# Kernel optimization log

Measured on AMD Instinct MI355X. Metric: run time of the kernel, lower is better.

## Reference

```python
import jax, jax.numpy as jnp
import numpy as np

EPS = 1e-6

def sparsemax(z):
    # z: [B, N]; sparsemax along last axis (Martins & Astudillo 2016)
    N = z.shape[-1]
    z_sorted = jnp.flip(jnp.sort(z, axis=-1), axis=-1)          # descending
    cs = jnp.cumsum(z_sorted, axis=-1)                            # [B, N]
    k = jnp.arange(1, N + 1, dtype=z.dtype)                       # [N]
    support = (1.0 + k * z_sorted) > cs                           # [B, N]
    k_sel = jnp.sum(support, axis=-1).astype(jnp.int32)           # [B]
    cs_k = jnp.take_along_axis(cs, (k_sel - 1)[:, None], axis=-1)[:, 0]
    tau = (cs_k - 1.0) / k_sel.astype(z.dtype)                    # [B]
    return jnp.maximum(z - tau[:, None], 0.0)

def _l2norm(x, axis):
    n = jnp.linalg.norm(x, axis=axis, keepdims=True)
    return x / jnp.maximum(n, EPS)

def setup_inputs() -> dict:
    key = jax.random.key(0)
    ks = jax.random.split(key, 6)
    B, N, D, OUT = 64, 4096, 1024, 1000
    D_IN, D_HID = 2 * D, 4 * D
    enc = jax.random.normal(ks[0], (B, D), dtype=jnp.float32)
    mem = jax.random.normal(ks[1], (B, N, D), dtype=jnp.float32)
    s1 = 1.0 / np.sqrt(D_IN)
    s2 = 1.0 / np.sqrt(D_HID)
    W1 = jax.random.uniform(ks[2], (D_HID, D_IN), jnp.float32, -s1, s1)
    b1 = jax.random.uniform(ks[3], (D_HID,), jnp.float32, -s1, s1)
    W2 = jax.random.uniform(ks[4], (OUT, D_HID), jnp.float32, -s2, s2)
    b2 = jax.random.uniform(ks[5], (OUT,), jnp.float32, -s2, s2)
    return {"encoder_output": enc, "memory_set": mem, "W1": W1, "b1": b1, "W2": W2, "b2": b2}

def reference(encoder_output, memory_set, W1, b1, W2, b2):
    # cosine distance: 1 - cos_sim
    xn = _l2norm(encoder_output, axis=-1)                         # [B, D]
    yn = _l2norm(memory_set, axis=-1)                             # [B, N, D]
    dist = 1.0 - jnp.einsum('bd,bnd->bn', xn, yn)                 # [B, N]
    content_weights = sparsemax(-dist)                            # [B, N]
    memory_vector = jnp.einsum('bn,bnd->bd', content_weights, memory_set)
    h = jnp.concatenate([encoder_output, memory_vector], axis=1)  # [B, 2D]
    h = jax.nn.relu(h @ W1.T + b1)
    return h @ W2.T + b2
```

## Files before the change

kernel.cpp:

```cpp
#include <hip/hip_runtime.h>
#include <cstdint>
#include <cstddef>

#define B_    64
#define N_    4096
#define D_    1024
#define DIN   2048
#define DHID  4096
#define OUT_N 1000
#define EPSF  1e-6f

__global__ void k_enc(const float* __restrict__ enc, float* __restrict__ cat,
                      float* __restrict__ inv_enc) {
  int b = blockIdx.x, tid = threadIdx.x;
  const float4* er = (const float4*)(enc + (size_t)b * D_);
  float4 v = er[tid];
  float ss = v.x*v.x + v.y*v.y + v.z*v.z + v.w*v.w;
  #pragma unroll
  for (int o = 32; o > 0; o >>= 1) ss += __shfl_xor(ss, o, 64);
  __shared__ float sb[4];
  if ((tid & 63) == 0) sb[tid >> 6] = ss;
  __syncthreads();
  if (tid == 0) {
    float t = sb[0] + sb[1] + sb[2] + sb[3];
    inv_enc[b] = 1.0f / fmaxf(sqrtf(t), EPSF);
  }
  ((float4*)(cat + (size_t)b * DIN))[tid] = v;
}

__global__ void k_cos(const float* __restrict__ enc, const float* __restrict__ mem,
                      const float* __restrict__ inv_enc, float* __restrict__ z) {
  int tid  = threadIdx.x;
  int lane = tid & 63;
  int r    = blockIdx.x * 4 + (tid >> 6);
  int b    = r >> 12;
  const float4* mr = (const float4*)mem + (size_t)r * 256;
  const float4* er = (const float4*)enc + (size_t)b * 256;
  float dot = 0.f, ss = 0.f;
  #pragma unroll
  for (int j = 0; j < 4; ++j) {
    float4 m = mr[j * 64 + lane];
    float4 e = er[j * 64 + lane];
    dot += e.x*m.x + e.y*m.y + e.z*m.z + e.w*m.w;
    ss  += m.x*m.x + m.y*m.y + m.z*m.z + m.w*m.w;
  }
  #pragma unroll
  for (int o = 32; o > 0; o >>= 1) {
    dot += __shfl_xor(dot, o, 64);
    ss  += __shfl_xor(ss,  o, 64);
  }
  if (lane == 0) z[r] = dot * inv_enc[b] / fmaxf(sqrtf(ss), EPSF);
}

__global__ void k_sparsemax(const float* __restrict__ z, int* __restrict__ idxl,
                            float* __restrict__ wl, int* __restrict__ cnt) {
  int b = blockIdx.x, tid = threadIdx.x;
  const float* zr = z + (size_t)b * N_;
  float zv[16];
  #pragma unroll
  for (int j = 0; j < 16; ++j) zv[j] = zr[j * 256 + tid];

  __shared__ float sb[4];
  __shared__ float sb2[4];

  float mx = -1e30f;
  #pragma unroll
  for (int j = 0; j < 16; ++j) mx = fmaxf(mx, zv[j]);
  #pragma unroll
  for (int o = 32; o > 0; o >>= 1) mx = fmaxf(mx, __shfl_xor(mx, o, 64));
  if ((tid & 63) == 0) sb[tid >> 6] = mx;
  __syncthreads();
  mx = fmaxf(fmaxf(sb[0], sb[1]), fmaxf(sb[2], sb[3]));
  __syncthreads();

  float lo = mx - 1.0f, hi = mx;
  for (int it = 0; it < 40; ++it) {
    float mid = 0.5f * (lo + hi);
    float s = 0.f;
    #pragma unroll
    for (int j = 0; j < 16; ++j) {
      float d = zv[j] - mid;
      s += (d > 0.f) ? d : 0.f;
    }
    #pragma unroll
    for (int o = 32; o > 0; o >>= 1) s += __shfl_xor(s, o, 64);
    if ((tid & 63) == 0) sb[tid >> 6] = s;
    __syncthreads();
    s = sb[0] + sb[1] + sb[2] + sb[3];
    __syncthreads();
    if (s >= 1.0f) lo = mid; else hi = mid;
  }
  float mid = 0.5f * (lo + hi);

  float c = 0.f, s = 0.f;
  #pragma unroll
  for (int j = 0; j < 16; ++j) {
    if (zv[j] > mid) { c += 1.0f; s += zv[j]; }
  }
  #pragma unroll
  for (int o = 32; o > 0; o >>= 1) {
    c += __shfl_xor(c, o, 64);
    s += __shfl_xor(s, o, 64);
  }
  if ((tid & 63) == 0) { sb[tid >> 6] = c; sb2[tid >> 6] = s; }
  __syncthreads();
  c = sb[0] + sb[1] + sb[2] + sb[3];
  s = sb2[0] + sb2[1] + sb2[2] + sb2[3];
  float tau = (s - 1.0f) / fmaxf(c, 1.0f);

  __shared__ int scnt;
  if (tid == 0) scnt = 0;
  __syncthreads();
  #pragma unroll
  for (int j = 0; j < 16; ++j) {
    float w = zv[j] - tau;
    if (w > 0.f) {
      int p = atomicAdd(&scnt, 1);
      idxl[(size_t)b * N_ + p] = j * 256 + tid;
      wl[(size_t)b * N_ + p]   = w;
    }
  }
  __syncthreads();
  if (tid == 0) cnt[b] = scnt;
}

__global__ void k_memvec(const float* __restrict__ mem, const int* __restrict__ idxl,
                         const float* __restrict__ wl, const int* __restrict__ cnt,
                         float* __restrict__ cat) {
  int b = blockIdx.x, tid = threadIdx.x;
  int nnz = cnt[b];
  __shared__ int   sidx[256];
  __shared__ float sw[256];
  float4 acc = make_float4(0.f, 0.f, 0.f, 0.f);
  const float4* mb = (const float4*)mem + (size_t)b * N_ * 256;
  for (int c0 = 0; c0 < nnz; c0 += 256) {
    int c = nnz - c0; if (c > 256) c = 256;
    if (tid < c) {
      sidx[tid] = idxl[(size_t)b * N_ + c0 + tid];
      sw[tid]   = wl[(size_t)b * N_ + c0 + tid];
    }
    __syncthreads();
    #pragma unroll 4
    for (int i = 0; i < c; ++i) {
      float  w = sw[i];
      float4 r = mb[(size_t)sidx[i] * 256 + tid];
      acc.x += w * r.x; acc.y += w * r.y; acc.z += w * r.z; acc.w += w * r.w;
    }
    __syncthreads();
  }
  ((float4*)(cat + (size_t)b * DIN + D_))[tid] = acc;
}

__global__ void k_gemm1(const float* __restrict__ X, const float* __restrict__ W,
                        float* __restrict__ hp) {
  int nt = blockIdx.x, kt = blockIdx.y, tid = threadIdx.x;
  __shared__ float Xs[16][68];
  __shared__ float Ws[16][68];
  int row = tid >> 2, c4 = (tid & 3) * 4;
  int tm = (tid & 15) * 4, tn = (tid >> 4) * 4;
  float acc[4][4] = {};
  const float* Xp = X + (size_t)row * DIN + c4;
  const float* Wp = W + ((size_t)nt * 64 + row) * DIN + c4;
  int kend = kt * 512 + 512;
  for (int k0 = kt * 512; k0 < kend; k0 += 16) {
    float4 xv = *(const float4*)(Xp + k0);
    float4 wv = *(const float4*)(Wp + k0);
    __syncthreads();
    Xs[c4+0][row] = xv.x; Xs[c4+1][row] = xv.y; Xs[c4+2][row] = xv.z; Xs[c4+3][row] = xv.w;
    Ws[c4+0][row] = wv.x; Ws[c4+1][row] = wv.y; Ws[c4+2][row] = wv.z; Ws[c4+3][row] = wv.w;
    __syncthreads();
    #pragma unroll
    for (int kk = 0; kk < 16; ++kk) {
      float a0 = Xs[kk][tm+0], a1 = Xs[kk][tm+1], a2 = Xs[kk][tm+2], a3 = Xs[kk][tm+3];
      float b0 = Ws[kk][tn+0], b1 = Ws[kk][tn+1], b2 = Ws[kk][tn+2], b3 = Ws[kk][tn+3];
      acc[0][0] += a0*b0; acc[0][1] += a0*b1; acc[0][2] += a0*b2; acc[0][3] += a0*b3;
      acc[1][0] += a1*b0; acc[1][1] += a1*b1; acc[1][2] += a1*b2; acc[1][3] += a1*b3;
      acc[2][0] += a2*b0; acc[2][1] += a2*b1; acc[2][2] += a2*b2; acc[2][3] += a2*b3;
      acc[3][0] += a3*b0; acc[3][1] += a3*b1; acc[3][2] += a3*b2; acc[3][3] += a3*b3;
    }
  }
  float* o = hp + ((size_t)kt * 64 + tm) * DHID + nt * 64 + tn;
  #pragma unroll
  for (int i = 0; i < 4; ++i)
    *(float4*)(o + (size_t)i * DHID) = make_float4(acc[i][0], acc[i][1], acc[i][2], acc[i][3]);
}

__global__ void k_gemm2(const float* __restrict__ hp, const float* __restrict__ b1p,
                        const float* __restrict__ W2, float* __restrict__ op) {
  int nt = blockIdx.x, kt = blockIdx.y, tid = threadIdx.x;
  __shared__ float Xs[16][68];
  __shared__ float Ws[16][68];
  int row = tid >> 2, c4 = (tid & 3) * 4;
  int tm = (tid & 15) * 4, tn = (tid >> 4) * 4;
  int nbase = nt * 64;
  float acc[4][4] = {};
  int kend = kt * 256 + 256;
  for (int k0 = kt * 256; k0 < kend; k0 += 16) {
    int k = k0 + c4;
    float4 xv = *(const float4*)(b1p + k);
    #pragma unroll
    for (int p = 0; p < 4; ++p) {
      float4 h = *(const float4*)(hp + ((size_t)p * 64 + row) * DHID + k);
      xv.x += h.x; xv.y += h.y; xv.z += h.z; xv.w += h.w;
    }
    xv.x = fmaxf(xv.x, 0.f); xv.y = fmaxf(xv.y, 0.f);
    xv.z = fmaxf(xv.z, 0.f); xv.w = fmaxf(xv.w, 0.f);
    int n = nbase + row;
    float4 wv = make_float4(0.f, 0.f, 0.f, 0.f);
    if (n < OUT_N) wv = *(const float4*)(W2 + (size_t)n * DHID + k);
    __syncthreads();
    Xs[c4+0][row] = xv.x; Xs[c4+1][row] = xv.y; Xs[c4+2][row] = xv.z; Xs[c4+3][row] = xv.w;
    Ws[c4+0][row] = wv.x; Ws[c4+1][row] = wv.y; Ws[c4+2][row] = wv.z; Ws[c4+3][row] = wv.w;
    __syncthreads();
    #pragma unroll
    for (int kk = 0; kk < 16; ++kk) {
      float a0 = Xs[kk][tm+0], a1 = Xs[kk][tm+1], a2 = Xs[kk][tm+2], a3 = Xs[kk][tm+3];
      float b0 = Ws[kk][tn+0], b1 = Ws[kk][tn+1], b2 = Ws[kk][tn+2], b3 = Ws[kk][tn+3];
      acc[0][0] += a0*b0; acc[0][1] += a0*b1; acc[0][2] += a0*b2; acc[0][3] += a0*b3;
      acc[1][0] += a1*b0; acc[1][1] += a1*b1; acc[1][2] += a1*b2; acc[1][3] += a1*b3;
      acc[2][0] += a2*b0; acc[2][1] += a2*b1; acc[2][2] += a2*b2; acc[2][3] += a2*b3;
      acc[3][0] += a3*b0; acc[3][1] += a3*b1; acc[3][2] += a3*b2; acc[3][3] += a3*b3;
    }
  }
  float* o = op + ((size_t)kt * 64 + tm) * 1024 + nbase + tn;
  #pragma unroll
  for (int i = 0; i < 4; ++i)
    *(float4*)(o + (size_t)i * 1024) = make_float4(acc[i][0], acc[i][1], acc[i][2], acc[i][3]);
}

__global__ void k_out(const float* __restrict__ op, const float* __restrict__ b2p,
                      float* __restrict__ out) {
  int o = blockIdx.x * 256 + threadIdx.x;
  int b = blockIdx.y;
  if (o >= OUT_N) return;
  float s = b2p[o];
  #pragma unroll
  for (int kt = 0; kt < 16; ++kt) s += op[((size_t)kt * 64 + b) * 1024 + o];
  out[(size_t)b * OUT_N + o] = s;
}

extern "C" void kernel_launch(void* const* d_in, const int* in_sizes, int n_in,
                              void* d_out, int out_size, void* d_ws, size_t ws_size,
                              hipStream_t stream) {
  const float* enc = (const float*)d_in[0];
  const float* mem = (const float*)d_in[1];
  const float* W1  = (const float*)d_in[2];
  const float* b1  = (const float*)d_in[3];
  const float* W2  = (const float*)d_in[4];
  const float* b2  = (const float*)d_in[5];
  float* out = (float*)d_out;

  float* ws      = (float*)d_ws;
  float* inv_enc = ws;
  int*   cnt     = (int*)(ws + 64);
  float* z       = ws + 128;
  int*   idxl    = (int*)(ws + 128 + 262144);
  float* wl      = ws + 128 + 2 * 262144;
  float* cat     = ws + 128 + 3 * 262144;
  float* hp      = cat + 131072;
  float* op      = hp + 1048576;

  k_enc      <<<dim3(64),      dim3(256), 0, stream>>>(enc, cat, inv_enc);
  k_cos      <<<dim3(65536),   dim3(256), 0, stream>>>(enc, mem, inv_enc, z);
  k_sparsemax<<<dim3(64),      dim3(256), 0, stream>>>(z, idxl, wl, cnt);
  k_memvec   <<<dim3(64),      dim3(256), 0, stream>>>(mem, idxl, wl, cnt, cat);
  k_gemm1    <<<dim3(64, 4),   dim3(256), 0, stream>>>(cat, W1, hp);
  k_gemm2    <<<dim3(16, 16),  dim3(256), 0, stream>>>(hp, b1, W2, op);
  k_out      <<<dim3(4, 64),   dim3(256), 0, stream>>>(op, b2, out);
}
```

Measured before the change: 1.423 ms.

## Split GEMM1 K further, add separate bias-ReLU reduce, move enc norm to sparsemax

GEMM1 now splits K into eight slices instead of four, doubling grid size for better occupancy, and a new kernel reduces the partials, adds bias and applies ReLU once. GEMM2 then reads the final hidden activations directly instead of re-reducing partials per tile. The cosine kernel uses rsqrt and drops the per-row inv_enc load, with the encoder norm scale applied in sparsemax instead. memvec unroll goes from 4 to 8. The costs are an extra launch and more partial-sum traffic, plus slightly different eps clamping semantics.

```diff
diff --git a/kernel.cpp b/kernel.cpp
--- a/kernel.cpp
+++ b/kernel.cpp
@@ -10,8 +10,8 @@
 #define OUT_N 1000
 #define EPSF  1e-6f
 
-__global__ void k_enc(const float* __restrict__ enc, float* __restrict__ cat,
-                      float* __restrict__ inv_enc) {
+__global__ void k_prep(const float* __restrict__ enc, float* __restrict__ cat,
+                       float* __restrict__ inv_enc) {
   int b = blockIdx.x, tid = threadIdx.x;
   const float4* er = (const float4*)(enc + (size_t)b * D_);
   float4 v = er[tid];
@@ -29,7 +29,7 @@
 }
 
 __global__ void k_cos(const float* __restrict__ enc, const float* __restrict__ mem,
-                      const float* __restrict__ inv_enc, float* __restrict__ z) {
+                      float* __restrict__ z) {
   int tid  = threadIdx.x;
   int lane = tid & 63;
   int r    = blockIdx.x * 4 + (tid >> 6);
@@ -49,16 +49,22 @@
     dot += __shfl_xor(dot, o, 64);
     ss  += __shfl_xor(ss,  o, 64);
   }
-  if (lane == 0) z[r] = dot * inv_enc[b] / fmaxf(sqrtf(ss), EPSF);
-}
-
-__global__ void k_sparsemax(const float* __restrict__ z, int* __restrict__ idxl,
-                            float* __restrict__ wl, int* __restrict__ cnt) {
+  if (lane == 0) {
+    float inv = rsqrtf(ss);
+    inv = fminf(inv, 1.0f / EPSF);
+    z[r] = dot * inv;
+  }
+}
+
+__global__ void k_sparsemax(const float* __restrict__ z, const float* __restrict__ inv_enc,
+                            int* __restrict__ idxl, float* __restrict__ wl,
+                            int* __restrict__ cnt) {
   int b = blockIdx.x, tid = threadIdx.x;
   const float* zr = z + (size_t)b * N_;
+  float ie = inv_enc[b];
   float zv[16];
   #pragma unroll
-  for (int j = 0; j < 16; ++j) zv[j] = zr[j * 256 + tid];
+  for (int j = 0; j < 16; ++j) zv[j] = zr[j * 256 + tid] * ie;
 
   __shared__ float sb[4];
   __shared__ float sb2[4];
@@ -140,7 +146,7 @@
       sw[tid]   = wl[(size_t)b * N_ + c0 + tid];
     }
     __syncthreads();
-    #pragma unroll 4
+    #pragma unroll 8
     for (int i = 0; i < c; ++i) {
       float  w = sw[i];
       float4 r = mb[(size_t)sidx[i] * 256 + tid];
@@ -161,8 +167,8 @@
   float acc[4][4] = {};
   const float* Xp = X + (size_t)row * DIN + c4;
   const float* Wp = W + ((size_t)nt * 64 + row) * DIN + c4;
-  int kend = kt * 512 + 512;
-  for (int k0 = kt * 512; k0 < kend; k0 += 16) {
+  int kend = kt * 256 + 256;
+  for (int k0 = kt * 256; k0 < kend; k0 += 16) {
     float4 xv = *(const float4*)(Xp + k0);
     float4 wv = *(const float4*)(Wp + k0);
     __syncthreads();
@@ -185,29 +191,38 @@
     *(float4*)(o + (size_t)i * DHID) = make_float4(acc[i][0], acc[i][1], acc[i][2], acc[i][3]);
 }
 
-__global__ void k_gemm2(const float* __restrict__ hp, const float* __restrict__ b1p,
-                        const float* __restrict__ W2, float* __restrict__ op) {
+__global__ void k_hrelu(const float* __restrict__ hp, const float* __restrict__ b1p,
+                        float* __restrict__ h) {
+  int flat4 = blockIdx.x * 256 + threadIdx.x;
+  int k4 = flat4 & 1023;
+  float4 acc = ((const float4*)b1p)[k4];
+  #pragma unroll
+  for (int p = 0; p < 8; ++p) {
+    float4 v = ((const float4*)hp)[(size_t)p * 65536 + flat4];
+    acc.x += v.x; acc.y += v.y; acc.z += v.z; acc.w += v.w;
+  }
+  acc.x = fmaxf(acc.x, 0.f); acc.y = fmaxf(acc.y, 0.f);
+  acc.z = fmaxf(acc.z, 0.f); acc.w = fmaxf(acc.w, 0.f);
+  ((float4*)h)[flat4] = acc;
+}
+
+__global__ void k_gemm2(const float* __restrict__ h, const float* __restrict__ W2,
+                        float* __restrict__ op) {
   int nt = blockIdx.x, kt = blockIdx.y, tid = threadIdx.x;
   __shared__ float Xs[16][68];
   __shared__ float Ws[16][68];
   int row = tid >> 2, c4 = (tid & 3) * 4;
   int tm = (tid & 15) * 4, tn = (tid >> 4) * 4;
   int nbase = nt * 64;
+  int n = nbase + row;
   float acc[4][4] = {};
+  const float* Xp = h + (size_t)row * DHID + c4;
+  const float* Wp = W2 + (size_t)n * DHID + c4;
   int kend = kt * 256 + 256;
   for (int k0 = kt * 256; k0 < kend; k0 += 16) {
-    int k = k0 + c4;
-    float4 xv = *(const float4*)(b1p + k);
-    #pragma unroll
-    for (int p = 0; p < 4; ++p) {
-      float4 h = *(const float4*)(hp + ((size_t)p * 64 + row) * DHID + k);
-      xv.x += h.x; xv.y += h.y; xv.z += h.z; xv.w += h.w;
-    }
-    xv.x = fmaxf(xv.x, 0.f); xv.y = fmaxf(xv.y, 0.f);
-    xv.z = fmaxf(xv.z, 0.f); xv.w = fmaxf(xv.w, 0.f);
-    int n = nbase + row;
+    float4 xv = *(const float4*)(Xp + k0);
     float4 wv = make_float4(0.f, 0.f, 0.f, 0.f);
-    if (n < OUT_N) wv = *(const float4*)(W2 + (size_t)n * DHID + k);
+    if (n < OUT_N) wv = *(const float4*)(Wp + k0);
     __syncthreads();
     Xs[c4+0][row] = xv.x; Xs[c4+1][row] = xv.y; Xs[c4+2][row] = xv.z; Xs[c4+3][row] = xv.w;
     Ws[c4+0][row] = wv.x; Ws[c4+1][row] = wv.y; Ws[c4+2][row] = wv.z; Ws[c4+3][row] = wv.w;
@@ -258,13 +273,15 @@
   float* wl      = ws + 128 + 2 * 262144;
   float* cat     = ws + 128 + 3 * 262144;
   float* hp      = cat + 131072;
-  float* op      = hp + 1048576;
-
-  k_enc      <<<dim3(64),      dim3(256), 0, stream>>>(enc, cat, inv_enc);
-  k_cos      <<<dim3(65536),   dim3(256), 0, stream>>>(enc, mem, inv_enc, z);
-  k_sparsemax<<<dim3(64),      dim3(256), 0, stream>>>(z, idxl, wl, cnt);
+  float* h       = hp + 2097152;
+  float* op      = h + 262144;
+
+  k_prep     <<<dim3(64),      dim3(256), 0, stream>>>(enc, cat, inv_enc);
+  k_cos      <<<dim3(65536),   dim3(256), 0, stream>>>(enc, mem, z);
+  k_sparsemax<<<dim3(64),      dim3(256), 0, stream>>>(z, inv_enc, idxl, wl, cnt);
   k_memvec   <<<dim3(64),      dim3(256), 0, stream>>>(mem, idxl, wl, cnt, cat);
-  k_gemm1    <<<dim3(64, 4),   dim3(256), 0, stream>>>(cat, W1, hp);
-  k_gemm2    <<<dim3(16, 16),  dim3(256), 0, stream>>>(hp, b1, W2, op);
+  k_gemm1    <<<dim3(64, 8),   dim3(256), 0, stream>>>(cat, W1, hp);
+  k_hrelu    <<<dim3(256),     dim3(256), 0, stream>>>(hp, b1, h);
+  k_gemm2    <<<dim3(16, 16),  dim3(256), 0, stream>>>(h, W2, op);
   k_out      <<<dim3(4, 64),   dim3(256), 0, stream>>>(op, b2, out);
 }
```

Result: no change. 1.421 ms (-0.2%).
